# Performance work log

Hardware: AMD Instinct MI355X
Metric: run time of the kernel (lower is better)

## Reference

```python
import jax, jax.numpy as jnp
import numpy as np

BETA = 1.0
K = 2.5
IOU_THRESH = 0.4


def point_form(boxes):
    # center form (cx, cy, w, h) -> corner form (xmin, ymin, xmax, ymax)
    return jnp.concatenate([boxes[:, :2] - boxes[:, 2:] / 2,
                            boxes[:, :2] + boxes[:, 2:] / 2], axis=1)


def jaccard(box_a, box_b):
    # box_a: [T,4], box_b: [P,4] corner form -> IoU [T,P]
    lt = jnp.maximum(box_a[:, None, :2], box_b[None, :, :2])
    rb = jnp.minimum(box_a[:, None, 2:], box_b[None, :, 2:])
    wh = jnp.clip(rb - lt, 0.0)
    inter = wh[..., 0] * wh[..., 1]  # [T,P]
    area_a = ((box_a[:, 2] - box_a[:, 0]) * (box_a[:, 3] - box_a[:, 1]))[:, None]
    area_b = ((box_b[:, 2] - box_b[:, 0]) * (box_b[:, 3] - box_b[:, 1]))[None, :]
    return inter / (area_a + area_b - inter)


def setup_inputs() -> dict:
    key = jax.random.key(0)
    k1, k2, k3, k4 = jax.random.split(key, 4)
    P, T = 262144, 128
    locs = jax.random.uniform(k1, (P, 2), dtype=jnp.float32)  # prior centers
    # params: (w, h, alpha_logit); keep w,h positive and modest
    wh = jax.random.uniform(k2, (P, 2), dtype=jnp.float32) * 0.2 + 0.02
    alpha = jax.random.normal(k3, (P, 1), dtype=jnp.float32)
    params = jnp.concatenate([wh, alpha], axis=1)
    # truths in corner form with positive extent
    t_cxcy = jax.random.uniform(k4, (T, 2), dtype=jnp.float32)
    t_wh = jax.random.uniform(jax.random.fold_in(key, 7), (T, 2), dtype=jnp.float32) * 0.3 + 0.1
    truths = jnp.concatenate([t_cxcy - t_wh / 2, t_cxcy + t_wh / 2], axis=1)
    # ensure every prior overlaps at least one truth (avoids log(0) degeneracy)
    truths = truths.at[0].set(jnp.array([0.0, 0.0, 1.0, 1.0], dtype=jnp.float32))
    return {"locs": locs, "params": params, "truths": truths}


def reference(locs, params, truths):
    sigmoid_alphas = jax.nn.sigmoid(params[:, -1])           # [P]
    priors = jnp.concatenate([locs, params[:, :2]], axis=1)  # [P,4] center form
    overlaps = jaccard(truths, point_form(priors))           # [T,P]
    best_truth_overlap = overlaps.max(axis=0)                # [P]
    best_prior_overlap = overlaps.max(axis=1)                # [T]
    best_prior_idx = overlaps.argmax(axis=1)                 # [T]
    best_truth_overlap = best_truth_overlap.at[best_prior_idx].set(best_prior_overlap)
    x_filter = jnp.where(best_truth_overlap > IOU_THRESH, 1.0, 0.0)
    x_filter = x_filter.at[best_prior_idx].set(K)
    loss = (-(sigmoid_alphas * x_filter * jnp.log(best_truth_overlap)).sum()
            + BETA * sigmoid_alphas.sum()) / x_filter.sum()
    return loss
```

## Files before the change

kernel.cpp:

```cpp
#include <hip/hip_runtime.h>

#define T_CNT   128
#define IOU_TH  0.4f
#define K_CONST 2.5f
#define PPB     256

static const size_t WS_ACC_OFF    = 0;
static const size_t WS_PACKED_OFF = 64;
static const size_t WS_BTO_OFF    = 4096;

__device__ inline float wave_max_dpp(float m) {
    int t;
    t = __builtin_amdgcn_update_dpp(__float_as_int(m), __float_as_int(m), 0x111, 0xf, 0xf, false);
    m = fmaxf(m, __int_as_float(t));
    t = __builtin_amdgcn_update_dpp(__float_as_int(m), __float_as_int(m), 0x112, 0xf, 0xf, false);
    m = fmaxf(m, __int_as_float(t));
    t = __builtin_amdgcn_update_dpp(__float_as_int(m), __float_as_int(m), 0x114, 0xf, 0xf, false);
    m = fmaxf(m, __int_as_float(t));
    t = __builtin_amdgcn_update_dpp(__float_as_int(m), __float_as_int(m), 0x118, 0xf, 0xf, false);
    m = fmaxf(m, __int_as_float(t));
    t = __builtin_amdgcn_update_dpp(__float_as_int(m), __float_as_int(m), 0x142, 0xa, 0xf, false);
    m = fmaxf(m, __int_as_float(t));
    t = __builtin_amdgcn_update_dpp(__float_as_int(m), __float_as_int(m), 0x143, 0xc, 0xf, false);
    m = fmaxf(m, __int_as_float(t));
    return m;
}

__global__ __launch_bounds__(256) void apb_single(
    const float* __restrict__ locs, const float* __restrict__ params,
    const float* __restrict__ truths, float* __restrict__ bto,
    unsigned long long* __restrict__ packed, double* __restrict__ accum)
{
    __shared__ float4 s_p[PPB];
    __shared__ unsigned long long s_part[4][T_CNT];
    __shared__ float s_red[3][4];

    const int tid  = threadIdx.x;
    const int lane = tid & 63;
    const int wv   = tid >> 6;
    const int base = blockIdx.x * PPB;

    {
        int p = base + tid;
        float2 c = ((const float2*)locs)[p];
        float w = params[3 * p];
        float h = params[3 * p + 1];
        s_p[tid] = make_float4(c.x - 0.5f * w, c.y - 0.5f * h,
                               c.x + 0.5f * w, c.y + 0.5f * h);
    }
    float4 t0 = ((const float4*)truths)[lane];
    float4 t1 = ((const float4*)truths)[64 + lane];
    float ta0 = (t0.z - t0.x) * (t0.w - t0.y);
    float ta1 = (t1.z - t1.x) * (t1.w - t1.y);
    __syncthreads();

    const int wbase = wv * 64;
    float maxv0 = -1.f, maxv1 = -1.f;
    unsigned int maxi0 = 0u, maxi1 = 0u;
    unsigned int b_bto = 0u;

#pragma unroll 4
    for (int j = 0; j < 64; ++j) {
        float4 pb = s_p[wbase + j];
        float parea = (pb.z - pb.x) * (pb.w - pb.y);
        unsigned int pg = (unsigned int)(base + wbase + j);

        float iou0, iou1;
        {
            float lx = fmaxf(t0.x, pb.x);
            float ly = fmaxf(t0.y, pb.y);
            float rx = fminf(t0.z, pb.z);
            float ry = fminf(t0.w, pb.w);
            float w = fmaxf(rx - lx, 0.f);
            float h = fmaxf(ry - ly, 0.f);
            float inter = w * h;
            iou0 = inter * __builtin_amdgcn_rcpf((ta0 + parea) - inter);
        }
        {
            float lx = fmaxf(t1.x, pb.x);
            float ly = fmaxf(t1.y, pb.y);
            float rx = fminf(t1.z, pb.z);
            float ry = fminf(t1.w, pb.w);
            float w = fmaxf(rx - lx, 0.f);
            float h = fmaxf(ry - ly, 0.f);
            float inter = w * h;
            iou1 = inter * __builtin_amdgcn_rcpf((ta1 + parea) - inter);
        }
        if (iou0 > maxv0) { maxv0 = iou0; maxi0 = pg; }
        if (iou1 > maxv1) { maxv1 = iou1; maxi1 = pg; }

        float m = wave_max_dpp(fmaxf(iou0, iou1));
        int r = __builtin_amdgcn_readlane(__float_as_int(m), 63);
        if (lane == j) b_bto = (unsigned int)r;
    }

    s_part[wv][lane] =
        ((unsigned long long)__float_as_uint(maxv0) << 32) |
        (unsigned long long)(~maxi0);
    s_part[wv][64 + lane] =
        ((unsigned long long)__float_as_uint(maxv1) << 32) |
        (unsigned long long)(~maxi1);

    const int q = base + wbase + lane;
    const float bt = __uint_as_float(b_bto);
    bto[q] = bt;
    float a = params[3 * q + 2];
    float sig = 1.f / (1.f + expf(-a));
    float xf = (bt > IOU_TH) ? 1.f : 0.f;
    float s1 = sig;
    float s2 = xf;
    float s3 = (xf > 0.f) ? sig * logf(bt) : 0.f;
#pragma unroll
    for (int off = 32; off; off >>= 1) {
        s1 += __shfl_xor(s1, off, 64);
        s2 += __shfl_xor(s2, off, 64);
        s3 += __shfl_xor(s3, off, 64);
    }
    if (lane == 0) { s_red[0][wv] = s1; s_red[1][wv] = s2; s_red[2][wv] = s3; }
    __syncthreads();

    if (tid < T_CNT) {
        unsigned long long m = s_part[0][tid];
        unsigned long long x1 = s_part[1][tid];
        unsigned long long x2 = s_part[2][tid];
        unsigned long long x3 = s_part[3][tid];
        m = (x1 > m) ? x1 : m;
        m = (x2 > m) ? x2 : m;
        m = (x3 > m) ? x3 : m;
        atomicMax(&packed[tid], m);
    }
    if (tid == 0) {
        atomicAdd(&accum[0], (double)(s_red[0][0] + s_red[0][1] + s_red[0][2] + s_red[0][3]));
        atomicAdd(&accum[1], (double)(s_red[1][0] + s_red[1][1] + s_red[1][2] + s_red[1][3]));
        atomicAdd(&accum[2], (double)(s_red[2][0] + s_red[2][1] + s_red[2][2] + s_red[2][3]));
    }
}

__global__ __launch_bounds__(128) void apb_final(
    const float* __restrict__ params, const float* __restrict__ bto,
    const unsigned long long* __restrict__ packed,
    const double* __restrict__ accum, float* __restrict__ out)
{
    const int t = threadIdx.x;
    __shared__ unsigned int s_idx[T_CNT];

    unsigned long long v = packed[t];
    float ov = __uint_as_float((unsigned int)(v >> 32));
    unsigned int p = ~(unsigned int)(v & 0xFFFFFFFFull);
    s_idx[t] = p;
    __syncthreads();

    bool is_last = true;
    for (int u = t + 1; u < T_CNT; ++u)
        if (s_idx[u] == p) is_last = false;

    float c2 = 0.f, c3 = 0.f;
    if (is_last && v != 0ull) {
        float old = bto[p];
        float oxf = (old > IOU_TH) ? 1.f : 0.f;
        float a = params[3 * p + 2];
        float sig = 1.f / (1.f + expf(-a));
        float oldterm = (oxf > 0.f) ? sig * logf(old) : 0.f;
        float newterm = K_CONST * sig * logf(ov);
        c3 = newterm - oldterm;
        c2 = K_CONST - oxf;
    }

#pragma unroll
    for (int off = 32; off; off >>= 1) {
        c2 += __shfl_xor(c2, off, 64);
        c3 += __shfl_xor(c3, off, 64);
    }
    __shared__ float sw[4];
    if ((t & 63) == 0) { sw[(t >> 6) * 2] = c2; sw[(t >> 6) * 2 + 1] = c3; }
    __syncthreads();

    if (t == 0) {
        double S1 = accum[0];
        double S2 = accum[1] + (double)(sw[0] + sw[2]);
        double S3 = accum[2] + (double)(sw[1] + sw[3]);
        out[0] = (float)((S1 - S3) / S2);
    }
}

extern "C" void kernel_launch(void* const* d_in, const int* in_sizes, int n_in,
                              void* d_out, int out_size, void* d_ws, size_t ws_size,
                              hipStream_t stream) {
    const float* locs   = (const float*)d_in[0];
    const float* params = (const float*)d_in[1];
    const float* truths = (const float*)d_in[2];
    const int P = in_sizes[0] / 2;

    double* accum = (double*)((char*)d_ws + WS_ACC_OFF);
    unsigned long long* packed = (unsigned long long*)((char*)d_ws + WS_PACKED_OFF);
    float* bto = (float*)((char*)d_ws + WS_BTO_OFF);

    (void)hipMemsetAsync(d_ws, 0, 1088, stream);

    apb_single<<<P / PPB, 256, 0, stream>>>(locs, params, truths, bto, packed, accum);
    apb_final<<<1, 128, 0, stream>>>(params, bto, packed, accum, (float*)d_out);
}
```

Baseline: 65.60 us.

## Split blocks into per-prior and per-truth roles and fuse final kernel via ticket

Launches twice as many blocks, with half computing each prior's best-truth IoU by looping over all truths (no cross-lane DPP reduction) and half computing per-truth argmax over prior chunks. The separate finalize kernel is folded into the last block through an atomic completion ticket with threadfences. This removes the per-iteration wave max reduction and a kernel launch, at the cost of computing the IoU matrix twice and hardcoding the block count to the problem size.

```diff
diff --git a/kernel.cpp b/kernel.cpp
--- a/kernel.cpp
+++ b/kernel.cpp
@@ -3,182 +3,198 @@
 #define T_CNT   128
 #define IOU_TH  0.4f
 #define K_CONST 2.5f
+#define NB_TOT  2048
 #define PPB     256
 
 static const size_t WS_ACC_OFF    = 0;
 static const size_t WS_PACKED_OFF = 64;
+static const size_t WS_DONE_OFF   = 1152;
 static const size_t WS_BTO_OFF    = 4096;
 
-__device__ inline float wave_max_dpp(float m) {
-    int t;
-    t = __builtin_amdgcn_update_dpp(__float_as_int(m), __float_as_int(m), 0x111, 0xf, 0xf, false);
-    m = fmaxf(m, __int_as_float(t));
-    t = __builtin_amdgcn_update_dpp(__float_as_int(m), __float_as_int(m), 0x112, 0xf, 0xf, false);
-    m = fmaxf(m, __int_as_float(t));
-    t = __builtin_amdgcn_update_dpp(__float_as_int(m), __float_as_int(m), 0x114, 0xf, 0xf, false);
-    m = fmaxf(m, __int_as_float(t));
-    t = __builtin_amdgcn_update_dpp(__float_as_int(m), __float_as_int(m), 0x118, 0xf, 0xf, false);
-    m = fmaxf(m, __int_as_float(t));
-    t = __builtin_amdgcn_update_dpp(__float_as_int(m), __float_as_int(m), 0x142, 0xa, 0xf, false);
-    m = fmaxf(m, __int_as_float(t));
-    t = __builtin_amdgcn_update_dpp(__float_as_int(m), __float_as_int(m), 0x143, 0xc, 0xf, false);
-    m = fmaxf(m, __int_as_float(t));
-    return m;
-}
-
-__global__ __launch_bounds__(256) void apb_single(
+__global__ __launch_bounds__(256) void apb_work(
     const float* __restrict__ locs, const float* __restrict__ params,
     const float* __restrict__ truths, float* __restrict__ bto,
-    unsigned long long* __restrict__ packed, double* __restrict__ accum)
+    unsigned long long* __restrict__ packed, double* __restrict__ accum,
+    unsigned int* __restrict__ done, float* __restrict__ out)
 {
+    __shared__ float4 s_tb[T_CNT];
     __shared__ float4 s_p[PPB];
     __shared__ unsigned long long s_part[4][T_CNT];
     __shared__ float s_red[3][4];
+    __shared__ unsigned int s_idx[T_CNT];
+    __shared__ float s_sw[8];
+    __shared__ unsigned int s_ticket;
 
     const int tid  = threadIdx.x;
     const int lane = tid & 63;
     const int wv   = tid >> 6;
-    const int base = blockIdx.x * PPB;
-
-    {
-        int p = base + tid;
+    const int bid  = blockIdx.x;
+    const int chunk = (bid >> 4) * 8 + (bid & 7);
+    const bool roleB = (bid >> 3) & 1;
+    const int base  = chunk * PPB;
+
+    if (!roleB) {
+        if (tid < T_CNT) s_tb[tid] = ((const float4*)truths)[tid];
+        __syncthreads();
+
+        const int p = base + tid;
         float2 c = ((const float2*)locs)[p];
-        float w = params[3 * p];
-        float h = params[3 * p + 1];
-        s_p[tid] = make_float4(c.x - 0.5f * w, c.y - 0.5f * h,
-                               c.x + 0.5f * w, c.y + 0.5f * h);
-    }
-    float4 t0 = ((const float4*)truths)[lane];
-    float4 t1 = ((const float4*)truths)[64 + lane];
-    float ta0 = (t0.z - t0.x) * (t0.w - t0.y);
-    float ta1 = (t1.z - t1.x) * (t1.w - t1.y);
-    __syncthreads();
-
-    const int wbase = wv * 64;
-    float maxv0 = -1.f, maxv1 = -1.f;
-    unsigned int maxi0 = 0u, maxi1 = 0u;
-    unsigned int b_bto = 0u;
-
+        float w0 = params[3 * p];
+        float h0 = params[3 * p + 1];
+        const float px1 = c.x - 0.5f * w0, py1 = c.y - 0.5f * h0;
+        const float px2 = c.x + 0.5f * w0, py2 = c.y + 0.5f * h0;
+        const float parea = (px2 - px1) * (py2 - py1);
+
+        float btmax = 0.f;
 #pragma unroll 4
-    for (int j = 0; j < 64; ++j) {
-        float4 pb = s_p[wbase + j];
-        float parea = (pb.z - pb.x) * (pb.w - pb.y);
-        unsigned int pg = (unsigned int)(base + wbase + j);
-
-        float iou0, iou1;
-        {
-            float lx = fmaxf(t0.x, pb.x);
-            float ly = fmaxf(t0.y, pb.y);
-            float rx = fminf(t0.z, pb.z);
-            float ry = fminf(t0.w, pb.w);
+        for (int t = 0; t < T_CNT; ++t) {
+            float4 tb = s_tb[t];
+            float ta = (tb.z - tb.x) * (tb.w - tb.y);
+            float lx = fmaxf(tb.x, px1);
+            float ly = fmaxf(tb.y, py1);
+            float rx = fminf(tb.z, px2);
+            float ry = fminf(tb.w, py2);
             float w = fmaxf(rx - lx, 0.f);
             float h = fmaxf(ry - ly, 0.f);
             float inter = w * h;
-            iou0 = inter * __builtin_amdgcn_rcpf((ta0 + parea) - inter);
-        }
-        {
-            float lx = fmaxf(t1.x, pb.x);
-            float ly = fmaxf(t1.y, pb.y);
-            float rx = fminf(t1.z, pb.z);
-            float ry = fminf(t1.w, pb.w);
-            float w = fmaxf(rx - lx, 0.f);
-            float h = fmaxf(ry - ly, 0.f);
-            float inter = w * h;
-            iou1 = inter * __builtin_amdgcn_rcpf((ta1 + parea) - inter);
-        }
-        if (iou0 > maxv0) { maxv0 = iou0; maxi0 = pg; }
-        if (iou1 > maxv1) { maxv1 = iou1; maxi1 = pg; }
-
-        float m = wave_max_dpp(fmaxf(iou0, iou1));
-        int r = __builtin_amdgcn_readlane(__float_as_int(m), 63);
-        if (lane == j) b_bto = (unsigned int)r;
-    }
-
-    s_part[wv][lane] =
-        ((unsigned long long)__float_as_uint(maxv0) << 32) |
-        (unsigned long long)(~maxi0);
-    s_part[wv][64 + lane] =
-        ((unsigned long long)__float_as_uint(maxv1) << 32) |
-        (unsigned long long)(~maxi1);
-
-    const int q = base + wbase + lane;
-    const float bt = __uint_as_float(b_bto);
-    bto[q] = bt;
-    float a = params[3 * q + 2];
-    float sig = 1.f / (1.f + expf(-a));
-    float xf = (bt > IOU_TH) ? 1.f : 0.f;
-    float s1 = sig;
-    float s2 = xf;
-    float s3 = (xf > 0.f) ? sig * logf(bt) : 0.f;
-#pragma unroll
-    for (int off = 32; off; off >>= 1) {
-        s1 += __shfl_xor(s1, off, 64);
-        s2 += __shfl_xor(s2, off, 64);
-        s3 += __shfl_xor(s3, off, 64);
-    }
-    if (lane == 0) { s_red[0][wv] = s1; s_red[1][wv] = s2; s_red[2][wv] = s3; }
-    __syncthreads();
-
-    if (tid < T_CNT) {
-        unsigned long long m = s_part[0][tid];
-        unsigned long long x1 = s_part[1][tid];
-        unsigned long long x2 = s_part[2][tid];
-        unsigned long long x3 = s_part[3][tid];
-        m = (x1 > m) ? x1 : m;
-        m = (x2 > m) ? x2 : m;
-        m = (x3 > m) ? x3 : m;
-        atomicMax(&packed[tid], m);
-    }
-    if (tid == 0) {
-        atomicAdd(&accum[0], (double)(s_red[0][0] + s_red[0][1] + s_red[0][2] + s_red[0][3]));
-        atomicAdd(&accum[1], (double)(s_red[1][0] + s_red[1][1] + s_red[1][2] + s_red[1][3]));
-        atomicAdd(&accum[2], (double)(s_red[2][0] + s_red[2][1] + s_red[2][2] + s_red[2][3]));
-    }
-}
-
-__global__ __launch_bounds__(128) void apb_final(
-    const float* __restrict__ params, const float* __restrict__ bto,
-    const unsigned long long* __restrict__ packed,
-    const double* __restrict__ accum, float* __restrict__ out)
-{
-    const int t = threadIdx.x;
-    __shared__ unsigned int s_idx[T_CNT];
-
-    unsigned long long v = packed[t];
-    float ov = __uint_as_float((unsigned int)(v >> 32));
-    unsigned int p = ~(unsigned int)(v & 0xFFFFFFFFull);
-    s_idx[t] = p;
-    __syncthreads();
-
-    bool is_last = true;
-    for (int u = t + 1; u < T_CNT; ++u)
-        if (s_idx[u] == p) is_last = false;
-
-    float c2 = 0.f, c3 = 0.f;
-    if (is_last && v != 0ull) {
-        float old = bto[p];
-        float oxf = (old > IOU_TH) ? 1.f : 0.f;
+            float iou = inter * __builtin_amdgcn_rcpf((ta + parea) - inter);
+            btmax = fmaxf(btmax, iou);
+        }
+
+        bto[p] = btmax;
         float a = params[3 * p + 2];
         float sig = 1.f / (1.f + expf(-a));
-        float oldterm = (oxf > 0.f) ? sig * logf(old) : 0.f;
-        float newterm = K_CONST * sig * logf(ov);
-        c3 = newterm - oldterm;
-        c2 = K_CONST - oxf;
-    }
-
+        float xf = (btmax > IOU_TH) ? 1.f : 0.f;
+        float s1 = sig;
+        float s2 = xf;
+        float s3 = (xf > 0.f) ? sig * logf(btmax) : 0.f;
+#pragma unroll
+        for (int off = 32; off; off >>= 1) {
+            s1 += __shfl_xor(s1, off, 64);
+            s2 += __shfl_xor(s2, off, 64);
+            s3 += __shfl_xor(s3, off, 64);
+        }
+        if (lane == 0) { s_red[0][wv] = s1; s_red[1][wv] = s2; s_red[2][wv] = s3; }
+        __syncthreads();
+        if (tid == 0) {
+            atomicAdd(&accum[0], (double)(s_red[0][0] + s_red[0][1] + s_red[0][2] + s_red[0][3]));
+            atomicAdd(&accum[1], (double)(s_red[1][0] + s_red[1][1] + s_red[1][2] + s_red[1][3]));
+            atomicAdd(&accum[2], (double)(s_red[2][0] + s_red[2][1] + s_red[2][2] + s_red[2][3]));
+        }
+    } else {
+        {
+            int p = base + tid;
+            float2 c = ((const float2*)locs)[p];
+            float w = params[3 * p];
+            float h = params[3 * p + 1];
+            s_p[tid] = make_float4(c.x - 0.5f * w, c.y - 0.5f * h,
+                                   c.x + 0.5f * w, c.y + 0.5f * h);
+        }
+        float4 t0 = ((const float4*)truths)[lane];
+        float4 t1 = ((const float4*)truths)[64 + lane];
+        float ta0 = (t0.z - t0.x) * (t0.w - t0.y);
+        float ta1 = (t1.z - t1.x) * (t1.w - t1.y);
+        __syncthreads();
+
+        const int wbase = wv * 64;
+        float maxv0 = -1.f, maxv1 = -1.f;
+        unsigned int maxi0 = 0u, maxi1 = 0u;
+
+#pragma unroll 4
+        for (int j = 0; j < 64; ++j) {
+            float4 pb = s_p[wbase + j];
+            float parea = (pb.z - pb.x) * (pb.w - pb.y);
+            unsigned int pg = (unsigned int)(base + wbase + j);
+            {
+                float lx = fmaxf(t0.x, pb.x);
+                float ly = fmaxf(t0.y, pb.y);
+                float rx = fminf(t0.z, pb.z);
+                float ry = fminf(t0.w, pb.w);
+                float w = fmaxf(rx - lx, 0.f);
+                float h = fmaxf(ry - ly, 0.f);
+                float inter = w * h;
+                float iou = inter * __builtin_amdgcn_rcpf((ta0 + parea) - inter);
+                if (iou > maxv0) { maxv0 = iou; maxi0 = pg; }
+            }
+            {
+                float lx = fmaxf(t1.x, pb.x);
+                float ly = fmaxf(t1.y, pb.y);
+                float rx = fminf(t1.z, pb.z);
+                float ry = fminf(t1.w, pb.w);
+                float w = fmaxf(rx - lx, 0.f);
+                float h = fmaxf(ry - ly, 0.f);
+                float inter = w * h;
+                float iou = inter * __builtin_amdgcn_rcpf((ta1 + parea) - inter);
+                if (iou > maxv1) { maxv1 = iou; maxi1 = pg; }
+            }
+        }
+
+        s_part[wv][lane] =
+            ((unsigned long long)__float_as_uint(maxv0) << 32) |
+            (unsigned long long)(~maxi0);
+        s_part[wv][64 + lane] =
+            ((unsigned long long)__float_as_uint(maxv1) << 32) |
+            (unsigned long long)(~maxi1);
+        __syncthreads();
+
+        if (tid < T_CNT) {
+            unsigned long long m = s_part[0][tid];
+            unsigned long long x1 = s_part[1][tid];
+            unsigned long long x2 = s_part[2][tid];
+            unsigned long long x3 = s_part[3][tid];
+            m = (x1 > m) ? x1 : m;
+            m = (x2 > m) ? x2 : m;
+            m = (x3 > m) ? x3 : m;
+            atomicMax(&packed[tid], m);
+        }
+    }
+
+    __threadfence();
+    __syncthreads();
+    if (tid == 0) s_ticket = atomicAdd(done, 1u);
+    __syncthreads();
+    if (s_ticket != NB_TOT - 1) return;
+
+    __threadfence();
+    unsigned long long v = 0ull;
+    float ov = 0.f;
+    unsigned int pi = 0u;
+    if (tid < T_CNT) {
+        v = packed[tid];
+        ov = __uint_as_float((unsigned int)(v >> 32));
+        pi = ~(unsigned int)(v & 0xFFFFFFFFull);
+        s_idx[tid] = pi;
+    }
+    __syncthreads();
+
+    float c2 = 0.f, c3 = 0.f;
+    if (tid < T_CNT) {
+        bool is_last = true;
+        for (int u = tid + 1; u < T_CNT; ++u)
+            if (s_idx[u] == pi) is_last = false;
+        if (is_last && v != 0ull) {
+            float old = bto[pi];
+            float oxf = (old > IOU_TH) ? 1.f : 0.f;
+            float a = params[3 * pi + 2];
+            float sig = 1.f / (1.f + expf(-a));
+            float oldterm = (oxf > 0.f) ? sig * logf(old) : 0.f;
+            float newterm = K_CONST * sig * logf(ov);
+            c3 = newterm - oldterm;
+            c2 = K_CONST - oxf;
+        }
+    }
 #pragma unroll
     for (int off = 32; off; off >>= 1) {
         c2 += __shfl_xor(c2, off, 64);
         c3 += __shfl_xor(c3, off, 64);
     }
-    __shared__ float sw[4];
-    if ((t & 63) == 0) { sw[(t >> 6) * 2] = c2; sw[(t >> 6) * 2 + 1] = c3; }
-    __syncthreads();
-
-    if (t == 0) {
+    if (lane == 0) { s_sw[wv * 2] = c2; s_sw[wv * 2 + 1] = c3; }
+    __syncthreads();
+
+    if (tid == 0) {
         double S1 = accum[0];
-        double S2 = accum[1] + (double)(sw[0] + sw[2]);
-        double S3 = accum[2] + (double)(sw[1] + sw[3]);
+        double S2 = accum[1] + (double)(s_sw[0] + s_sw[2]);
+        double S3 = accum[2] + (double)(s_sw[1] + s_sw[3]);
         out[0] = (float)((S1 - S3) / S2);
     }
 }
@@ -189,14 +205,14 @@
     const float* locs   = (const float*)d_in[0];
     const float* params = (const float*)d_in[1];
     const float* truths = (const float*)d_in[2];
-    const int P = in_sizes[0] / 2;
 
     double* accum = (double*)((char*)d_ws + WS_ACC_OFF);
     unsigned long long* packed = (unsigned long long*)((char*)d_ws + WS_PACKED_OFF);
+    unsigned int* done = (unsigned int*)((char*)d_ws + WS_DONE_OFF);
     float* bto = (float*)((char*)d_ws + WS_BTO_OFF);
 
-    (void)hipMemsetAsync(d_ws, 0, 1088, stream);
-
-    apb_single<<<P / PPB, 256, 0, stream>>>(locs, params, truths, bto, packed, accum);
-    apb_final<<<1, 128, 0, stream>>>(params, bto, packed, accum, (float*)d_out);
+    (void)hipMemsetAsync(d_ws, 0, 2048, stream);
+
+    apb_work<<<NB_TOT, 256, 0, stream>>>(locs, params, truths, bto, packed,
+                                         accum, done, (float*)d_out);
 }
```

Measured after the change: 145.0 us. 2.21x slower.

## Replace per-prior DPP wave reductions with shared-memory transpose reduction

Applied to the files above, without the earlier changes.

The per-prior column max over all 128 truths was a 6-step DPP reduction plus readlane for each of the 64 priors per wave. It is replaced by a transposed reduction: each wave writes 16 priors' max IoUs to LDS, then each lane reduces a 16-element segment with a rotated index to avoid bank conflicts and finishes with two xor shuffles. This removes the serial cross-lane chains from the inner loop. In exchange it adds LDS traffic, 16 KB of extra shared memory per block that may lower occupancy, and relies on wave-synchronous LDS ordering with no explicit barrier.

```diff
diff --git a/kernel.cpp b/kernel.cpp
--- a/kernel.cpp
+++ b/kernel.cpp
@@ -4,34 +4,19 @@
 #define IOU_TH  0.4f
 #define K_CONST 2.5f
 #define PPB     256
+#define QP      16
 
 static const size_t WS_ACC_OFF    = 0;
 static const size_t WS_PACKED_OFF = 64;
 static const size_t WS_BTO_OFF    = 4096;
 
-__device__ inline float wave_max_dpp(float m) {
-    int t;
-    t = __builtin_amdgcn_update_dpp(__float_as_int(m), __float_as_int(m), 0x111, 0xf, 0xf, false);
-    m = fmaxf(m, __int_as_float(t));
-    t = __builtin_amdgcn_update_dpp(__float_as_int(m), __float_as_int(m), 0x112, 0xf, 0xf, false);
-    m = fmaxf(m, __int_as_float(t));
-    t = __builtin_amdgcn_update_dpp(__float_as_int(m), __float_as_int(m), 0x114, 0xf, 0xf, false);
-    m = fmaxf(m, __int_as_float(t));
-    t = __builtin_amdgcn_update_dpp(__float_as_int(m), __float_as_int(m), 0x118, 0xf, 0xf, false);
-    m = fmaxf(m, __int_as_float(t));
-    t = __builtin_amdgcn_update_dpp(__float_as_int(m), __float_as_int(m), 0x142, 0xa, 0xf, false);
-    m = fmaxf(m, __int_as_float(t));
-    t = __builtin_amdgcn_update_dpp(__float_as_int(m), __float_as_int(m), 0x143, 0xc, 0xf, false);
-    m = fmaxf(m, __int_as_float(t));
-    return m;
-}
-
-__global__ __launch_bounds__(256) void apb_single(
+__global__ __launch_bounds__(256) void apb_fused(
     const float* __restrict__ locs, const float* __restrict__ params,
     const float* __restrict__ truths, float* __restrict__ bto,
     unsigned long long* __restrict__ packed, double* __restrict__ accum)
 {
     __shared__ float4 s_p[PPB];
+    __shared__ float  s_m[4][QP][64];
     __shared__ unsigned long long s_part[4][T_CNT];
     __shared__ float s_red[3][4];
 
@@ -57,41 +42,52 @@
     const int wbase = wv * 64;
     float maxv0 = -1.f, maxv1 = -1.f;
     unsigned int maxi0 = 0u, maxi1 = 0u;
-    unsigned int b_bto = 0u;
+    float btsel = 0.f;
+    const int j0  = lane & 15;
+    const int seg = lane >> 4;
 
-#pragma unroll 4
-    for (int j = 0; j < 64; ++j) {
-        float4 pb = s_p[wbase + j];
-        float parea = (pb.z - pb.x) * (pb.w - pb.y);
-        unsigned int pg = (unsigned int)(base + wbase + j);
+    for (int qtr = 0; qtr < 4; ++qtr) {
+#pragma unroll
+        for (int jj = 0; jj < QP; ++jj) {
+            const int j = qtr * QP + jj;
+            float4 pb = s_p[wbase + j];
+            float parea = (pb.z - pb.x) * (pb.w - pb.y);
+            unsigned int pg = (unsigned int)(base + wbase + j);
 
-        float iou0, iou1;
-        {
-            float lx = fmaxf(t0.x, pb.x);
-            float ly = fmaxf(t0.y, pb.y);
-            float rx = fminf(t0.z, pb.z);
-            float ry = fminf(t0.w, pb.w);
-            float w = fmaxf(rx - lx, 0.f);
-            float h = fmaxf(ry - ly, 0.f);
-            float inter = w * h;
-            iou0 = inter * __builtin_amdgcn_rcpf((ta0 + parea) - inter);
+            float iou0, iou1;
+            {
+                float lx = fmaxf(t0.x, pb.x);
+                float ly = fmaxf(t0.y, pb.y);
+                float rx = fminf(t0.z, pb.z);
+                float ry = fminf(t0.w, pb.w);
+                float w = fmaxf(rx - lx, 0.f);
+                float h = fmaxf(ry - ly, 0.f);
+                float inter = w * h;
+                iou0 = inter * __builtin_amdgcn_rcpf((ta0 + parea) - inter);
+            }
+            {
+                float lx = fmaxf(t1.x, pb.x);
+                float ly = fmaxf(t1.y, pb.y);
+                float rx = fminf(t1.z, pb.z);
+                float ry = fminf(t1.w, pb.w);
+                float w = fmaxf(rx - lx, 0.f);
+                float h = fmaxf(ry - ly, 0.f);
+                float inter = w * h;
+                iou1 = inter * __builtin_amdgcn_rcpf((ta1 + parea) - inter);
+            }
+            if (iou0 > maxv0) { maxv0 = iou0; maxi0 = pg; }
+            if (iou1 > maxv1) { maxv1 = iou1; maxi1 = pg; }
+            s_m[wv][jj][lane] = fmaxf(iou0, iou1);
         }
-        {
-            float lx = fmaxf(t1.x, pb.x);
-            float ly = fmaxf(t1.y, pb.y);
-            float rx = fminf(t1.z, pb.z);
-            float ry = fminf(t1.w, pb.w);
-            float w = fmaxf(rx - lx, 0.f);
-            float h = fmaxf(ry - ly, 0.f);
-            float inter = w * h;
-            iou1 = inter * __builtin_amdgcn_rcpf((ta1 + parea) - inter);
+        float m = -1.f;
+#pragma unroll
+        for (int k = 0; k < QP; ++k) {
+            int kk = (k + j0) & 15;
+            m = fmaxf(m, s_m[wv][j0][seg * 16 + kk]);
         }
-        if (iou0 > maxv0) { maxv0 = iou0; maxi0 = pg; }
-        if (iou1 > maxv1) { maxv1 = iou1; maxi1 = pg; }
-
-        float m = wave_max_dpp(fmaxf(iou0, iou1));
-        int r = __builtin_amdgcn_readlane(__float_as_int(m), 63);
-        if (lane == j) b_bto = (unsigned int)r;
+        m = fmaxf(m, __shfl_xor(m, 16, 64));
+        m = fmaxf(m, __shfl_xor(m, 32, 64));
+        if (seg == qtr) btsel = m;
     }
 
     s_part[wv][lane] =
@@ -102,14 +98,13 @@
         (unsigned long long)(~maxi1);
 
     const int q = base + wbase + lane;
-    const float bt = __uint_as_float(b_bto);
-    bto[q] = bt;
+    bto[q] = btsel;
     float a = params[3 * q + 2];
     float sig = 1.f / (1.f + expf(-a));
-    float xf = (bt > IOU_TH) ? 1.f : 0.f;
+    float xf = (btsel > IOU_TH) ? 1.f : 0.f;
     float s1 = sig;
     float s2 = xf;
-    float s3 = (xf > 0.f) ? sig * logf(bt) : 0.f;
+    float s3 = (xf > 0.f) ? sig * logf(btsel) : 0.f;
 #pragma unroll
     for (int off = 32; off; off >>= 1) {
         s1 += __shfl_xor(s1, off, 64);
@@ -197,6 +192,6 @@
 
     (void)hipMemsetAsync(d_ws, 0, 1088, stream);
 
-    apb_single<<<P / PPB, 256, 0, stream>>>(locs, params, truths, bto, packed, accum);
+    apb_fused<<<P / PPB, 256, 0, stream>>>(locs, params, truths, bto, packed, accum);
     apb_final<<<1, 128, 0, stream>>>(params, bto, packed, accum, (float*)d_out);
 }
```

Result: faster. 63.55 us (-3.1%).

## Compute per-prior best overlap in a separate pass instead of DPP wave reductions

Applied to the files above, without the earlier changes.

Replaces the per-iteration 64-lane DPP max reduction used to build each prior's best truth overlap with a separate loop in which every thread loops over all 128 truths for its own prior. Truths and prior areas are staged in shared memory. This removes the cross-lane shuffle chain and readlane from the inner loop, but computes every IoU twice (once per prior pass, once per truth pass). The grid size is also hardcoded to 1024 blocks, which matches the test problem size only.

```diff
diff --git a/kernel.cpp b/kernel.cpp
--- a/kernel.cpp
+++ b/kernel.cpp
@@ -4,34 +4,21 @@
 #define IOU_TH  0.4f
 #define K_CONST 2.5f
 #define PPB     256
+#define NBLK    1024
 
 static const size_t WS_ACC_OFF    = 0;
 static const size_t WS_PACKED_OFF = 64;
 static const size_t WS_BTO_OFF    = 4096;
 
-__device__ inline float wave_max_dpp(float m) {
-    int t;
-    t = __builtin_amdgcn_update_dpp(__float_as_int(m), __float_as_int(m), 0x111, 0xf, 0xf, false);
-    m = fmaxf(m, __int_as_float(t));
-    t = __builtin_amdgcn_update_dpp(__float_as_int(m), __float_as_int(m), 0x112, 0xf, 0xf, false);
-    m = fmaxf(m, __int_as_float(t));
-    t = __builtin_amdgcn_update_dpp(__float_as_int(m), __float_as_int(m), 0x114, 0xf, 0xf, false);
-    m = fmaxf(m, __int_as_float(t));
-    t = __builtin_amdgcn_update_dpp(__float_as_int(m), __float_as_int(m), 0x118, 0xf, 0xf, false);
-    m = fmaxf(m, __int_as_float(t));
-    t = __builtin_amdgcn_update_dpp(__float_as_int(m), __float_as_int(m), 0x142, 0xa, 0xf, false);
-    m = fmaxf(m, __int_as_float(t));
-    t = __builtin_amdgcn_update_dpp(__float_as_int(m), __float_as_int(m), 0x143, 0xc, 0xf, false);
-    m = fmaxf(m, __int_as_float(t));
-    return m;
-}
-
-__global__ __launch_bounds__(256) void apb_single(
+__global__ __launch_bounds__(256) void apb_work(
     const float* __restrict__ locs, const float* __restrict__ params,
     const float* __restrict__ truths, float* __restrict__ bto,
     unsigned long long* __restrict__ packed, double* __restrict__ accum)
 {
+    __shared__ float4 s_tb[T_CNT];
+    __shared__ float  s_ta[T_CNT];
     __shared__ float4 s_p[PPB];
+    __shared__ float  s_pa[PPB];
     __shared__ unsigned long long s_part[4][T_CNT];
     __shared__ float s_red[3][4];
 
@@ -40,32 +27,51 @@
     const int wv   = tid >> 6;
     const int base = blockIdx.x * PPB;
 
-    {
-        int p = base + tid;
-        float2 c = ((const float2*)locs)[p];
-        float w = params[3 * p];
-        float h = params[3 * p + 1];
-        s_p[tid] = make_float4(c.x - 0.5f * w, c.y - 0.5f * h,
-                               c.x + 0.5f * w, c.y + 0.5f * h);
-    }
-    float4 t0 = ((const float4*)truths)[lane];
-    float4 t1 = ((const float4*)truths)[64 + lane];
-    float ta0 = (t0.z - t0.x) * (t0.w - t0.y);
-    float ta1 = (t1.z - t1.x) * (t1.w - t1.y);
-    __syncthreads();
-
+    const int p = base + tid;
+    float2 c = ((const float2*)locs)[p];
+    float w0 = params[3 * p];
+    float h0 = params[3 * p + 1];
+    const float4 pc = make_float4(c.x - 0.5f * w0, c.y - 0.5f * h0,
+                                  c.x + 0.5f * w0, c.y + 0.5f * h0);
+    const float parea = (pc.z - pc.x) * (pc.w - pc.y);
+    s_p[tid]  = pc;
+    s_pa[tid] = parea;
+    if (tid < T_CNT) {
+        float4 tb = ((const float4*)truths)[tid];
+        s_tb[tid] = tb;
+        s_ta[tid] = (tb.z - tb.x) * (tb.w - tb.y);
+    }
+    __syncthreads();
+
+    float btmax = 0.f;
+#pragma unroll 4
+    for (int t = 0; t < T_CNT; ++t) {
+        float4 tb = s_tb[t];
+        float ta = s_ta[t];
+        float lx = fmaxf(tb.x, pc.x);
+        float ly = fmaxf(tb.y, pc.y);
+        float rx = fminf(tb.z, pc.z);
+        float ry = fminf(tb.w, pc.w);
+        float w = fmaxf(rx - lx, 0.f);
+        float h = fmaxf(ry - ly, 0.f);
+        float inter = w * h;
+        float iou = inter * __builtin_amdgcn_rcpf((ta + parea) - inter);
+        btmax = fmaxf(btmax, iou);
+    }
+
+    float4 t0 = s_tb[lane];
+    float4 t1 = s_tb[64 + lane];
+    float ta0 = s_ta[lane];
+    float ta1 = s_ta[64 + lane];
     const int wbase = wv * 64;
+
     float maxv0 = -1.f, maxv1 = -1.f;
     unsigned int maxi0 = 0u, maxi1 = 0u;
-    unsigned int b_bto = 0u;
-
 #pragma unroll 4
     for (int j = 0; j < 64; ++j) {
         float4 pb = s_p[wbase + j];
-        float parea = (pb.z - pb.x) * (pb.w - pb.y);
+        float pa = s_pa[wbase + j];
         unsigned int pg = (unsigned int)(base + wbase + j);
-
-        float iou0, iou1;
         {
             float lx = fmaxf(t0.x, pb.x);
             float ly = fmaxf(t0.y, pb.y);
@@ -74,7 +80,8 @@
             float w = fmaxf(rx - lx, 0.f);
             float h = fmaxf(ry - ly, 0.f);
             float inter = w * h;
-            iou0 = inter * __builtin_amdgcn_rcpf((ta0 + parea) - inter);
+            float iou = inter * __builtin_amdgcn_rcpf((ta0 + pa) - inter);
+            if (iou > maxv0) { maxv0 = iou; maxi0 = pg; }
         }
         {
             float lx = fmaxf(t1.x, pb.x);
@@ -84,14 +91,9 @@
             float w = fmaxf(rx - lx, 0.f);
             float h = fmaxf(ry - ly, 0.f);
             float inter = w * h;
-            iou1 = inter * __builtin_amdgcn_rcpf((ta1 + parea) - inter);
+            float iou = inter * __builtin_amdgcn_rcpf((ta1 + pa) - inter);
+            if (iou > maxv1) { maxv1 = iou; maxi1 = pg; }
         }
-        if (iou0 > maxv0) { maxv0 = iou0; maxi0 = pg; }
-        if (iou1 > maxv1) { maxv1 = iou1; maxi1 = pg; }
-
-        float m = wave_max_dpp(fmaxf(iou0, iou1));
-        int r = __builtin_amdgcn_readlane(__float_as_int(m), 63);
-        if (lane == j) b_bto = (unsigned int)r;
     }
 
     s_part[wv][lane] =
@@ -101,15 +103,13 @@
         ((unsigned long long)__float_as_uint(maxv1) << 32) |
         (unsigned long long)(~maxi1);
 
-    const int q = base + wbase + lane;
-    const float bt = __uint_as_float(b_bto);
-    bto[q] = bt;
-    float a = params[3 * q + 2];
+    bto[p] = btmax;
+    float a = params[3 * p + 2];
     float sig = 1.f / (1.f + expf(-a));
-    float xf = (bt > IOU_TH) ? 1.f : 0.f;
+    float xf = (btmax > IOU_TH) ? 1.f : 0.f;
     float s1 = sig;
     float s2 = xf;
-    float s3 = (xf > 0.f) ? sig * logf(bt) : 0.f;
+    float s3 = (xf > 0.f) ? sig * logf(btmax) : 0.f;
 #pragma unroll
     for (int off = 32; off; off >>= 1) {
         s1 += __shfl_xor(s1, off, 64);
@@ -189,7 +189,6 @@
     const float* locs   = (const float*)d_in[0];
     const float* params = (const float*)d_in[1];
     const float* truths = (const float*)d_in[2];
-    const int P = in_sizes[0] / 2;
 
     double* accum = (double*)((char*)d_ws + WS_ACC_OFF);
     unsigned long long* packed = (unsigned long long*)((char*)d_ws + WS_PACKED_OFF);
@@ -197,6 +196,6 @@
 
     (void)hipMemsetAsync(d_ws, 0, 1088, stream);
 
-    apb_single<<<P / PPB, 256, 0, stream>>>(locs, params, truths, bto, packed, accum);
+    apb_work<<<NBLK, 256, 0, stream>>>(locs, params, truths, bto, packed, accum);
     apb_final<<<1, 128, 0, stream>>>(params, bto, packed, accum, (float*)d_out);
 }
```

Measured after the change: 67.72 us. 1.03x slower.
